# Kernel optimization log

Hardware: AMD Instinct MI355X
Metric: run time of the kernel (lower is better)

## Reference

```python
import jax, jax.numpy as jnp
import numpy as np

NB_HEAD = 16
SIZE_PER_HEAD = 64
D_MODEL = NB_HEAD * SIZE_PER_HEAD  # 1024
B, L = 2, 2048
NEG_BIG = 1e12


def setup_inputs() -> dict:
    key = jax.random.key(0)
    ks = jax.random.split(key, 8)
    return {
        "Q_seq": jax.random.normal(ks[0], (B, L, D_MODEL), dtype=jnp.float32),
        "K_seq": jax.random.normal(ks[1], (B, L, D_MODEL), dtype=jnp.float32),
        "V_seq": jax.random.normal(ks[2], (B, L, D_MODEL), dtype=jnp.float32),
        "q_len": jax.random.randint(ks[3], (B, 1), 1, L, dtype=jnp.int32),
        "v_len": jax.random.randint(ks[4], (B, 1), 1, L, dtype=jnp.int32),
        "WQ": jax.random.normal(ks[5], (D_MODEL, D_MODEL), dtype=jnp.float32) * 0.02,
        "WK": jax.random.normal(ks[6], (D_MODEL, D_MODEL), dtype=jnp.float32) * 0.02,
        "WV": jax.random.normal(ks[7], (D_MODEL, D_MODEL), dtype=jnp.float32) * 0.02,
    }


def _len_mask(lens, length, dtype):
    # Keras code: mask = 1 - cumsum(one_hot(len, L)) -> 1 for pos < len, 0 otherwise
    return (jnp.arange(length)[None, :] < lens).astype(dtype)  # [B, L]


def reference(Q_seq, K_seq, V_seq, q_len, v_len, WQ, WK, WV):
    Bq, Lq, _ = Q_seq.shape
    Lk = K_seq.shape[1]
    # QKV projections, split heads: [B, H, L, D]
    q = (Q_seq @ WQ).reshape(Bq, Lq, NB_HEAD, SIZE_PER_HEAD).transpose(0, 2, 1, 3)
    k = (K_seq @ WK).reshape(Bq, Lk, NB_HEAD, SIZE_PER_HEAD).transpose(0, 2, 1, 3)
    v = (V_seq @ WV).reshape(Bq, Lk, NB_HEAD, SIZE_PER_HEAD).transpose(0, 2, 1, 3)
    # scaled dot-product scores [B, H, Lq, Lk]
    scores = jnp.einsum("bhqd,bhkd->bhqk", q, k) / np.float32(SIZE_PER_HEAD ** 0.5)
    # additive key-length mask (V_len), matching Mask(..., 'add')
    kmask = _len_mask(v_len, Lk, scores.dtype)  # [B, Lk]
    scores = scores - (1.0 - kmask)[:, None, None, :] * np.float32(NEG_BIG)
    A = jax.nn.softmax(scores, axis=-1)
    # attention output, merge heads: [B, Lq, H*D]
    O = jnp.einsum("bhqk,bhkd->bqhd", A, v).reshape(Bq, Lq, D_MODEL)
    # multiplicative query-length mask (Q_len), matching Mask(..., 'mul')
    qmask = _len_mask(q_len, Lq, O.dtype)  # [B, Lq]
    return O * qmask[:, :, None]
```

## Files before the change

kernel.cpp:

```cpp
#include <hip/hip_runtime.h>
#include <cstddef>

#define NB_HEAD 16
#define HEAD_DIM 64
#define D_MODEL 1024
#define BATCH 2
#define SEQ 2048
#define MROWS (BATCH * SEQ)

typedef __bf16 bf16x8 __attribute__((ext_vector_type(8)));
typedef __bf16 bf16x4 __attribute__((ext_vector_type(4)));
typedef float  f32x4  __attribute__((ext_vector_type(4)));

#define XEL ((size_t)MROWS * D_MODEL)
#define WEL ((size_t)D_MODEL * D_MODEL)

static __device__ __forceinline__ size_t xchunk(int row, int k) {
    return ((size_t)(row >> 4) * 32 + (k >> 5)) * 512 + ((k >> 3) & 3) * 128 + (row & 15) * 8 + (k & 7);
}
static __device__ __forceinline__ size_t qkbase(int bh, int row16, int dc) {
    return ((size_t)(bh * 128 + row16) * 2 + dc) * 512;
}
static __device__ __forceinline__ size_t qkelem(int bh, int row, int d) {
    return qkbase(bh, row >> 4, d >> 5) + ((d >> 3) & 3) * 128 + (row & 15) * 8 + (d & 7);
}
static __device__ __forceinline__ size_t vbase(int bh, int d16, int kc) {
    return ((size_t)(bh * 4 + d16) * 64 + kc) * 512;
}
static __device__ __forceinline__ size_t velem(int bh, int d, int key) {
    return vbase(bh, d >> 4, key >> 5) + ((key >> 3) & 3) * 128 + (d & 15) * 8 + (key & 7);
}

static __device__ __forceinline__ void split_bf16(float x, __bf16& h, __bf16& l) {
    h = (__bf16)x;
    l = (__bf16)(x - (float)h);
}

__global__ __launch_bounds__(256) void conv_wt_kernel(
    const float* __restrict__ W0, const float* __restrict__ W1,
    const float* __restrict__ W2,
    __bf16* __restrict__ hi, __bf16* __restrict__ lo)
{
    __shared__ float tile[64][65];
    const int t  = threadIdx.x;
    const int k0 = blockIdx.x * 64;
    const int n0 = blockIdx.y * 64;
    const int z  = blockIdx.z;
    const float* W = (z == 0) ? W0 : ((z == 1) ? W1 : W2);
    __bf16* hz = hi + (size_t)z * WEL;
    __bf16* lz = lo + (size_t)z * WEL;

    #pragma unroll
    for (int p = 0; p < 4; ++p) {
        const int e = (p * 256 + t) * 4;
        const int r = e >> 6, c = e & 63;
        const float4 v = *(const float4*)(W + (size_t)(k0 + r) * D_MODEL + n0 + c);
        tile[r][c] = v.x; tile[r][c + 1] = v.y; tile[r][c + 2] = v.z; tile[r][c + 3] = v.w;
    }
    __syncthreads();
    #pragma unroll
    for (int p = 0; p < 4; ++p) {
        const int e = (p * 256 + t) * 4;
        const int n = e >> 6, kc = e & 63;
        __bf16 h[4], l[4];
        #pragma unroll
        for (int u = 0; u < 4; ++u) split_bf16(tile[kc + u][n], h[u], l[u]);
        const size_t a = xchunk(n0 + n, k0 + kc);
        *(bf16x4*)(hz + a) = (bf16x4){h[0], h[1], h[2], h[3]};
        *(bf16x4*)(lz + a) = (bf16x4){l[0], l[1], l[2], l[3]};
    }
}

__global__ __launch_bounds__(256) void conv_x_kernel(
    const float* __restrict__ X0, const float* __restrict__ X1,
    const float* __restrict__ X2,
    const int* __restrict__ q_len, const int* __restrict__ v_len,
    __bf16* __restrict__ xhi, __bf16* __restrict__ xlo)
{
    const int z = blockIdx.y;
    const size_t e = ((size_t)blockIdx.x * 256 + threadIdx.x) * 8;
    const int l = (int)(e >> 10), k = (int)(e & 1023);
    const int bb = l >> 11, lb = l & (SEQ - 1);
    const int len = (z == 0) ? q_len[bb] : v_len[bb];
    if (lb >= ((len + 127) & ~127)) return;

    const float* X = (z == 0) ? X0 : ((z == 1) ? X1 : X2);
    const float4 v0 = *(const float4*)(X + e);
    const float4 v1 = *(const float4*)(X + e + 4);
    const float xs[8] = {v0.x, v0.y, v0.z, v0.w, v1.x, v1.y, v1.z, v1.w};
    bf16x8 h8, l8;
    #pragma unroll
    for (int u = 0; u < 8; ++u) { __bf16 h_, l_; split_bf16(xs[u], h_, l_); h8[u] = h_; l8[u] = l_; }
    const size_t a = z * XEL + xchunk(l, k);
    *(bf16x8*)(xhi + a) = h8;
    *(bf16x8*)(xlo + a) = l8;
}

__global__ __launch_bounds__(256, 2) void proj_mfma_kernel(
    const __bf16* __restrict__ Xhi, const __bf16* __restrict__ Xlo,
    const __bf16* __restrict__ Wchi, const __bf16* __restrict__ Wclo,
    const int* __restrict__ q_len, const int* __restrict__ v_len,
    __bf16* __restrict__ qch, __bf16* __restrict__ qcl,
    __bf16* __restrict__ kch, __bf16* __restrict__ kcl,
    __bf16* __restrict__ vch, __bf16* __restrict__ vcl)
{
    const int t    = threadIdx.x;
    const int wave = t >> 6, lane = t & 63;
    const int li   = lane & 15, grp = lane >> 4;
    const int wm   = wave >> 1, wn = wave & 1;
    const int m0   = blockIdx.x * 128;
    const int n0   = blockIdx.y * 128;
    const int z    = blockIdx.z;
    const int bb   = m0 >> 11;
    const int l0   = m0 & (SEQ - 1);
    const int need = (z == 0) ? q_len[bb] : v_len[bb];
    if (l0 >= need) return;

    const __bf16* Xh = Xhi + z * XEL;
    const __bf16* Xl = Xlo + z * XEL;
    const __bf16* Wh = Wchi + z * WEL;
    const __bf16* Wl = Wclo + z * WEL;

    const size_t abase = ((size_t)((m0 >> 4) + wm * 4) * 32) * 512 + lane * 8;
    const size_t bbase = ((size_t)((n0 >> 4) + wn * 4) * 32) * 512 + lane * 8;

    f32x4 acc[4][4] = {};
    bf16x8 ah[2][4], al[2][4], bh[2][4], bl[2][4];

    #pragma unroll
    for (int i = 0; i < 4; ++i) {
        ah[0][i] = *(const bf16x8*)(Xh + abase + (size_t)i * 16384);
        al[0][i] = *(const bf16x8*)(Xl + abase + (size_t)i * 16384);
        bh[0][i] = *(const bf16x8*)(Wh + bbase + (size_t)i * 16384);
        bl[0][i] = *(const bf16x8*)(Wl + bbase + (size_t)i * 16384);
    }

    #pragma unroll 2
    for (int kc = 0; kc < 32; ++kc) {
        const int cur = kc & 1, nxt = cur ^ 1;
        if (kc < 31) {
            const size_t ka = abase + (size_t)(kc + 1) * 512;
            const size_t kb = bbase + (size_t)(kc + 1) * 512;
            #pragma unroll
            for (int i = 0; i < 4; ++i) {
                ah[nxt][i] = *(const bf16x8*)(Xh + ka + (size_t)i * 16384);
                al[nxt][i] = *(const bf16x8*)(Xl + ka + (size_t)i * 16384);
                bh[nxt][i] = *(const bf16x8*)(Wh + kb + (size_t)i * 16384);
                bl[nxt][i] = *(const bf16x8*)(Wl + kb + (size_t)i * 16384);
            }
        }
        #pragma unroll
        for (int j = 0; j < 4; ++j) {
            #pragma unroll
            for (int i = 0; i < 4; ++i) {
                acc[i][j] = __builtin_amdgcn_mfma_f32_16x16x32_bf16(ah[cur][i], bh[cur][j], acc[i][j], 0, 0, 0);
                acc[i][j] = __builtin_amdgcn_mfma_f32_16x16x32_bf16(ah[cur][i], bl[cur][j], acc[i][j], 0, 0, 0);
                acc[i][j] = __builtin_amdgcn_mfma_f32_16x16x32_bf16(al[cur][i], bh[cur][j], acc[i][j], 0, 0, 0);
            }
        }
    }

    #pragma unroll
    for (int j = 0; j < 4; ++j) {
        const int cg = n0 + wn * 64 + j * 16 + li;
        const int hd = cg >> 6, d = cg & 63;
        const int bhI = bb * NB_HEAD + hd;
        #pragma unroll
        for (int i = 0; i < 4; ++i) {
            #pragma unroll
            for (int r = 0; r < 4; ++r) {
                const int rg = m0 + wm * 64 + i * 16 + grp * 4 + r;
                const int lg = rg & (SEQ - 1);
                __bf16 h_, l_;
                split_bf16(acc[i][j][r], h_, l_);
                if (z == 0) {
                    const size_t a = qkelem(bhI, lg, d);
                    qch[a] = h_; qcl[a] = l_;
                } else if (z == 1) {
                    const size_t a = qkelem(bhI, lg, d);
                    kch[a] = h_; kcl[a] = l_;
                } else {
                    const size_t a = velem(bhI, d, lg);
                    vch[a] = h_; vcl[a] = l_;
                }
            }
        }
    }
}

__global__ __launch_bounds__(256, 2) void attn_mfma_kernel(
    const __bf16* __restrict__ qch, const __bf16* __restrict__ qcl,
    const __bf16* __restrict__ kch, const __bf16* __restrict__ kcl,
    const __bf16* __restrict__ vch, const __bf16* __restrict__ vcl,
    const int* __restrict__ q_len, const int* __restrict__ v_len,
    float* __restrict__ out)
{
    __shared__ __align__(16) __bf16 Ps[128][72];

    const int t = threadIdx.x;
    const int wq = t >> 6, lane = t & 63;
    const int grp = lane >> 4, li = lane & 15;
    const int hh = blockIdx.x;
    const int q0 = blockIdx.y * 128;
    const int b  = blockIdx.z;
    const int qlen = q_len[b], vlen = v_len[b];
    const int bh = b * NB_HEAD + hh;
    const int qbase = q0 + wq * 32;

    if (qbase >= qlen) {
        const int row = qbase + (lane >> 1), cs = (lane & 1) * 32;
        float* o = out + ((size_t)b * SEQ + row) * D_MODEL + hh * HEAD_DIM + cs;
        const float4 z4 = make_float4(0.f, 0.f, 0.f, 0.f);
        #pragma unroll
        for (int u = 0; u < 8; ++u) *(float4*)(o + u * 4) = z4;
        return;
    }

    bf16x8 qh[2][2], ql[2][2];
    #pragma unroll
    for (int s = 0; s < 2; ++s)
        #pragma unroll
        for (int ks = 0; ks < 2; ++ks) {
            const size_t a = qkbase(bh, (qbase >> 4) + s, ks) + lane * 8;
            qh[s][ks] = *(const bf16x8*)(qch + a);
            ql[s][ks] = *(const bf16x8*)(qcl + a);
        }

    f32x4 O[2][4] = {};
    float m_s[2][4], l_s[2][4];
    #pragma unroll
    for (int s = 0; s < 2; ++s)
        #pragma unroll
        for (int r = 0; r < 4; ++r) { m_s[s][r] = -1e30f; l_s[s][r] = 0.f; }

    const int nkt = (vlen + 63) >> 6;

    for (int tt = 0; tt < nkt; ++tt) {
        const int k0 = tt * 64;

        f32x4 sacc[2][4] = {};
        #pragma unroll
        for (int ks = 0; ks < 2; ++ks) {
            bf16x8 kh_[4], kl_[4];
            #pragma unroll
            for (int j = 0; j < 4; ++j) {
                const size_t a = qkbase(bh, (k0 >> 4) + j, ks) + lane * 8;
                kh_[j] = *(const bf16x8*)(kch + a);
                kl_[j] = *(const bf16x8*)(kcl + a);
            }
            #pragma unroll
            for (int j = 0; j < 4; ++j)
                #pragma unroll
                for (int s = 0; s < 2; ++s) {
                    sacc[s][j] = __builtin_amdgcn_mfma_f32_16x16x32_bf16(qh[s][ks], kh_[j], sacc[s][j], 0, 0, 0);
                    sacc[s][j] = __builtin_amdgcn_mfma_f32_16x16x32_bf16(qh[s][ks], kl_[j], sacc[s][j], 0, 0, 0);
                    sacc[s][j] = __builtin_amdgcn_mfma_f32_16x16x32_bf16(ql[s][ks], kh_[j], sacc[s][j], 0, 0, 0);
                }
        }

        bf16x8 vh_[2][4], vl_[2][4];
        #pragma unroll
        for (int ks = 0; ks < 2; ++ks)
            #pragma unroll
            for (int j = 0; j < 4; ++j) {
                const size_t a = vbase(bh, j, (k0 >> 5) + ks) + lane * 8;
                vh_[ks][j] = *(const bf16x8*)(vch + a);
                vl_[ks][j] = *(const bf16x8*)(vcl + a);
            }

        #pragma unroll
        for (int s = 0; s < 2; ++s) {
            float mx[4] = {-1e30f, -1e30f, -1e30f, -1e30f};
            #pragma unroll
            for (int j = 0; j < 4; ++j) {
                const int key = k0 + j * 16 + li;
                #pragma unroll
                for (int r = 0; r < 4; ++r) {
                    float v = sacc[s][j][r] * 0.125f;
                    if (key >= vlen) v = -1e30f;
                    sacc[s][j][r] = v;
                    mx[r] = fmaxf(mx[r], v);
                }
            }
            #pragma unroll
            for (int r = 0; r < 4; ++r) {
                mx[r] = fmaxf(mx[r], __shfl_xor(mx[r], 1));
                mx[r] = fmaxf(mx[r], __shfl_xor(mx[r], 2));
                mx[r] = fmaxf(mx[r], __shfl_xor(mx[r], 4));
                mx[r] = fmaxf(mx[r], __shfl_xor(mx[r], 8));
            }
            float al[4], sum[4];
            #pragma unroll
            for (int r = 0; r < 4; ++r) {
                const float mn = fmaxf(m_s[s][r], mx[r]);
                al[r] = __expf(m_s[s][r] - mn);
                m_s[s][r] = mn;
                sum[r] = 0.f;
            }
            #pragma unroll
            for (int j = 0; j < 4; ++j)
                #pragma unroll
                for (int r = 0; r < 4; ++r) {
                    const float p = __expf(sacc[s][j][r] - m_s[s][r]);
                    const __bf16 pb = (__bf16)p;
                    sum[r] += (float)pb;
                    Ps[wq * 32 + s * 16 + grp * 4 + r][j * 16 + li] = pb;
                }
            #pragma unroll
            for (int r = 0; r < 4; ++r) {
                sum[r] += __shfl_xor(sum[r], 1);
                sum[r] += __shfl_xor(sum[r], 2);
                sum[r] += __shfl_xor(sum[r], 4);
                sum[r] += __shfl_xor(sum[r], 8);
                l_s[s][r] = l_s[s][r] * al[r] + sum[r];
            }
            #pragma unroll
            for (int j = 0; j < 4; ++j)
                #pragma unroll
                for (int r = 0; r < 4; ++r) O[s][j][r] *= al[r];
        }
        asm volatile("s_waitcnt lgkmcnt(0)" ::: "memory");

        #pragma unroll
        for (int ks = 0; ks < 2; ++ks) {
            bf16x8 pa[2];
            #pragma unroll
            for (int s = 0; s < 2; ++s)
                pa[s] = *(const bf16x8*)&Ps[wq * 32 + s * 16 + li][ks * 32 + grp * 8];
            #pragma unroll
            for (int j = 0; j < 4; ++j)
                #pragma unroll
                for (int s = 0; s < 2; ++s) {
                    O[s][j] = __builtin_amdgcn_mfma_f32_16x16x32_bf16(pa[s], vh_[ks][j], O[s][j], 0, 0, 0);
                    O[s][j] = __builtin_amdgcn_mfma_f32_16x16x32_bf16(pa[s], vl_[ks][j], O[s][j], 0, 0, 0);
                }
        }
    }

    #pragma unroll
    for (int s = 0; s < 2; ++s)
        #pragma unroll
        for (int r = 0; r < 4; ++r) {
            const int q = qbase + s * 16 + grp * 4 + r;
            const float inv = (q < qlen) ? 1.f / l_s[s][r] : 0.f;
            #pragma unroll
            for (int j = 0; j < 4; ++j)
                out[((size_t)b * SEQ + q) * D_MODEL + hh * HEAD_DIM + j * 16 + li] = O[s][j][r] * inv;
        }
}

extern "C" void kernel_launch(void* const* d_in, const int* in_sizes, int n_in,
                              void* d_out, int out_size, void* d_ws, size_t ws_size,
                              hipStream_t stream)
{
    (void)in_sizes; (void)n_in; (void)out_size; (void)ws_size;
    const float* Q_seq = (const float*)d_in[0];
    const float* K_seq = (const float*)d_in[1];
    const float* V_seq = (const float*)d_in[2];
    const int*   q_len = (const int*)d_in[3];
    const int*   v_len = (const int*)d_in[4];
    const float* WQ    = (const float*)d_in[5];
    const float* WK    = (const float*)d_in[6];
    const float* WV    = (const float*)d_in[7];
    float* out = (float*)d_out;

    __bf16* wchi = (__bf16*)d_ws;
    __bf16* wclo = wchi + 3 * WEL;
    __bf16* xhi_ = wclo + 3 * WEL;
    __bf16* xlo_ = xhi_ + 3 * XEL;
    __bf16* qch_ = xlo_ + 3 * XEL;
    __bf16* qcl_ = qch_ + XEL;
    __bf16* kch_ = qcl_ + XEL;
    __bf16* kcl_ = kch_ + XEL;
    __bf16* vch_ = kcl_ + XEL;
    __bf16* vcl_ = vch_ + XEL;

    dim3 blk(256);

    dim3 cg(D_MODEL / 64, D_MODEL / 64, 3);
    conv_wt_kernel<<<cg, blk, 0, stream>>>(WQ, WK, WV, wchi, wclo);

    dim3 xg((unsigned)(XEL / 2048), 3);
    conv_x_kernel<<<xg, blk, 0, stream>>>(Q_seq, K_seq, V_seq, q_len, v_len, xhi_, xlo_);

    dim3 pg(MROWS / 128, D_MODEL / 128, 3);
    proj_mfma_kernel<<<pg, blk, 0, stream>>>(xhi_, xlo_, wchi, wclo, q_len, v_len,
                                             qch_, qcl_, kch_, kcl_, vch_, vcl_);

    dim3 ag(NB_HEAD, SEQ / 128, BATCH);
    attn_mfma_kernel<<<ag, blk, 0, stream>>>(qch_, qcl_, kch_, kcl_, vch_, vcl_,
                                             q_len, v_len, out);
}
```

Measured before the change: 304.5 us.

## Shrink projection M-tile, fold score scale into Q, widen attention key tile

The projection kernel now uses 64-row M tiles with a larger grid and launch bounds that request three blocks per SIMD, which should raise occupancy and parallelism. The 1/sqrt(d) scale moves into the Q projection epilogue, so the attention kernel no longer multiplies every score. The attention kernel processes 128 keys per iteration, skips key masking on full tiles, and loads K/V fragments just in time instead of staging arrays. It also drops the explicit LDS waitcnt, which risks a race on Ps unless the compiler inserts the wait itself.

```diff
diff --git a/kernel.cpp b/kernel.cpp
--- a/kernel.cpp
+++ b/kernel.cpp
@@ -79,7 +79,7 @@
 {
     const int z = blockIdx.y;
     const size_t e = ((size_t)blockIdx.x * 256 + threadIdx.x) * 8;
-    const int l = (int)(e >> 10), k = (int)(e & 1023);
+    const int l = (int)(e >> 10);
     const int bb = l >> 11, lb = l & (SEQ - 1);
     const int len = (z == 0) ? q_len[bb] : v_len[bb];
     if (lb >= ((len + 127) & ~127)) return;
@@ -91,12 +91,12 @@
     bf16x8 h8, l8;
     #pragma unroll
     for (int u = 0; u < 8; ++u) { __bf16 h_, l_; split_bf16(xs[u], h_, l_); h8[u] = h_; l8[u] = l_; }
-    const size_t a = z * XEL + xchunk(l, k);
+    const size_t a = z * XEL + xchunk(l, (int)(e & 1023));
     *(bf16x8*)(xhi + a) = h8;
     *(bf16x8*)(xlo + a) = l8;
 }
 
-__global__ __launch_bounds__(256, 2) void proj_mfma_kernel(
+__global__ __launch_bounds__(256, 3) void proj_mfma_kernel(
     const __bf16* __restrict__ Xhi, const __bf16* __restrict__ Xlo,
     const __bf16* __restrict__ Wchi, const __bf16* __restrict__ Wclo,
     const int* __restrict__ q_len, const int* __restrict__ v_len,
@@ -108,7 +108,7 @@
     const int wave = t >> 6, lane = t & 63;
     const int li   = lane & 15, grp = lane >> 4;
     const int wm   = wave >> 1, wn = wave & 1;
-    const int m0   = blockIdx.x * 128;
+    const int m0   = blockIdx.x * 64;
     const int n0   = blockIdx.y * 128;
     const int z    = blockIdx.z;
     const int bb   = m0 >> 11;
@@ -121,18 +121,21 @@
     const __bf16* Wh = Wchi + z * WEL;
     const __bf16* Wl = Wclo + z * WEL;
 
-    const size_t abase = ((size_t)((m0 >> 4) + wm * 4) * 32) * 512 + lane * 8;
+    const size_t abase = ((size_t)((m0 >> 4) + wm * 2) * 32) * 512 + lane * 8;
     const size_t bbase = ((size_t)((n0 >> 4) + wn * 4) * 32) * 512 + lane * 8;
 
-    f32x4 acc[4][4] = {};
-    bf16x8 ah[2][4], al[2][4], bh[2][4], bl[2][4];
-
-    #pragma unroll
-    for (int i = 0; i < 4; ++i) {
+    f32x4 acc[2][4] = {};
+    bf16x8 ah[2][2], al[2][2], bh[2][4], bl[2][4];
+
+    #pragma unroll
+    for (int i = 0; i < 2; ++i) {
         ah[0][i] = *(const bf16x8*)(Xh + abase + (size_t)i * 16384);
         al[0][i] = *(const bf16x8*)(Xl + abase + (size_t)i * 16384);
-        bh[0][i] = *(const bf16x8*)(Wh + bbase + (size_t)i * 16384);
-        bl[0][i] = *(const bf16x8*)(Wl + bbase + (size_t)i * 16384);
+    }
+    #pragma unroll
+    for (int j = 0; j < 4; ++j) {
+        bh[0][j] = *(const bf16x8*)(Wh + bbase + (size_t)j * 16384);
+        bl[0][j] = *(const bf16x8*)(Wl + bbase + (size_t)j * 16384);
     }
 
     #pragma unroll 2
@@ -142,37 +145,40 @@
             const size_t ka = abase + (size_t)(kc + 1) * 512;
             const size_t kb = bbase + (size_t)(kc + 1) * 512;
             #pragma unroll
-            for (int i = 0; i < 4; ++i) {
+            for (int i = 0; i < 2; ++i) {
                 ah[nxt][i] = *(const bf16x8*)(Xh + ka + (size_t)i * 16384);
                 al[nxt][i] = *(const bf16x8*)(Xl + ka + (size_t)i * 16384);
-                bh[nxt][i] = *(const bf16x8*)(Wh + kb + (size_t)i * 16384);
-                bl[nxt][i] = *(const bf16x8*)(Wl + kb + (size_t)i * 16384);
-            }
-        }
-        #pragma unroll
-        for (int j = 0; j < 4; ++j) {
-            #pragma unroll
-            for (int i = 0; i < 4; ++i) {
+            }
+            #pragma unroll
+            for (int j = 0; j < 4; ++j) {
+                bh[nxt][j] = *(const bf16x8*)(Wh + kb + (size_t)j * 16384);
+                bl[nxt][j] = *(const bf16x8*)(Wl + kb + (size_t)j * 16384);
+            }
+        }
+        #pragma unroll
+        for (int j = 0; j < 4; ++j)
+            #pragma unroll
+            for (int i = 0; i < 2; ++i) {
                 acc[i][j] = __builtin_amdgcn_mfma_f32_16x16x32_bf16(ah[cur][i], bh[cur][j], acc[i][j], 0, 0, 0);
                 acc[i][j] = __builtin_amdgcn_mfma_f32_16x16x32_bf16(ah[cur][i], bl[cur][j], acc[i][j], 0, 0, 0);
                 acc[i][j] = __builtin_amdgcn_mfma_f32_16x16x32_bf16(al[cur][i], bh[cur][j], acc[i][j], 0, 0, 0);
             }
-        }
-    }
-
+    }
+
+    const float oscale = (z == 0) ? 0.125f : 1.0f;
     #pragma unroll
     for (int j = 0; j < 4; ++j) {
         const int cg = n0 + wn * 64 + j * 16 + li;
         const int hd = cg >> 6, d = cg & 63;
         const int bhI = bb * NB_HEAD + hd;
         #pragma unroll
-        for (int i = 0; i < 4; ++i) {
+        for (int i = 0; i < 2; ++i) {
             #pragma unroll
             for (int r = 0; r < 4; ++r) {
-                const int rg = m0 + wm * 64 + i * 16 + grp * 4 + r;
+                const int rg = m0 + wm * 32 + i * 16 + grp * 4 + r;
                 const int lg = rg & (SEQ - 1);
                 __bf16 h_, l_;
-                split_bf16(acc[i][j][r], h_, l_);
+                split_bf16(acc[i][j][r] * oscale, h_, l_);
                 if (z == 0) {
                     const size_t a = qkelem(bhI, lg, d);
                     qch[a] = h_; qcl[a] = l_;
@@ -195,7 +201,7 @@
     const int* __restrict__ q_len, const int* __restrict__ v_len,
     float* __restrict__ out)
 {
-    __shared__ __align__(16) __bf16 Ps[128][72];
+    __shared__ __align__(16) __bf16 Ps[128][132];
 
     const int t = threadIdx.x;
     const int wq = t >> 6, lane = t & 63;
@@ -233,54 +239,49 @@
         #pragma unroll
         for (int r = 0; r < 4; ++r) { m_s[s][r] = -1e30f; l_s[s][r] = 0.f; }
 
-    const int nkt = (vlen + 63) >> 6;
+    const int nkt = (vlen + 127) >> 7;
 
     for (int tt = 0; tt < nkt; ++tt) {
-        const int k0 = tt * 64;
-
-        f32x4 sacc[2][4] = {};
+        const int k0 = tt * 128;
+        const bool full = (k0 + 128 <= vlen);
+
+        f32x4 sacc[2][8] = {};
         #pragma unroll
         for (int ks = 0; ks < 2; ++ks) {
-            bf16x8 kh_[4], kl_[4];
-            #pragma unroll
-            for (int j = 0; j < 4; ++j) {
+            #pragma unroll
+            for (int j = 0; j < 8; ++j) {
                 const size_t a = qkbase(bh, (k0 >> 4) + j, ks) + lane * 8;
-                kh_[j] = *(const bf16x8*)(kch + a);
-                kl_[j] = *(const bf16x8*)(kcl + a);
-            }
-            #pragma unroll
-            for (int j = 0; j < 4; ++j)
+                const bf16x8 kh_ = *(const bf16x8*)(kch + a);
+                const bf16x8 kl_ = *(const bf16x8*)(kcl + a);
                 #pragma unroll
                 for (int s = 0; s < 2; ++s) {
-                    sacc[s][j] = __builtin_amdgcn_mfma_f32_16x16x32_bf16(qh[s][ks], kh_[j], sacc[s][j], 0, 0, 0);
-                    sacc[s][j] = __builtin_amdgcn_mfma_f32_16x16x32_bf16(qh[s][ks], kl_[j], sacc[s][j], 0, 0, 0);
-                    sacc[s][j] = __builtin_amdgcn_mfma_f32_16x16x32_bf16(ql[s][ks], kh_[j], sacc[s][j], 0, 0, 0);
-                }
-        }
-
-        bf16x8 vh_[2][4], vl_[2][4];
-        #pragma unroll
-        for (int ks = 0; ks < 2; ++ks)
-            #pragma unroll
-            for (int j = 0; j < 4; ++j) {
-                const size_t a = vbase(bh, j, (k0 >> 5) + ks) + lane * 8;
-                vh_[ks][j] = *(const bf16x8*)(vch + a);
-                vl_[ks][j] = *(const bf16x8*)(vcl + a);
-            }
+                    sacc[s][j] = __builtin_amdgcn_mfma_f32_16x16x32_bf16(qh[s][ks], kh_, sacc[s][j], 0, 0, 0);
+                    sacc[s][j] = __builtin_amdgcn_mfma_f32_16x16x32_bf16(qh[s][ks], kl_, sacc[s][j], 0, 0, 0);
+                    sacc[s][j] = __builtin_amdgcn_mfma_f32_16x16x32_bf16(ql[s][ks], kh_, sacc[s][j], 0, 0, 0);
+                }
+            }
+        }
 
         #pragma unroll
         for (int s = 0; s < 2; ++s) {
             float mx[4] = {-1e30f, -1e30f, -1e30f, -1e30f};
-            #pragma unroll
-            for (int j = 0; j < 4; ++j) {
-                const int key = k0 + j * 16 + li;
-                #pragma unroll
-                for (int r = 0; r < 4; ++r) {
-                    float v = sacc[s][j][r] * 0.125f;
-                    if (key >= vlen) v = -1e30f;
-                    sacc[s][j][r] = v;
-                    mx[r] = fmaxf(mx[r], v);
-                }
+            if (!full) {
+                #pragma unroll
+                for (int j = 0; j < 8; ++j) {
+                    const int key = k0 + j * 16 + li;
+                    #pragma unroll
+                    for (int r = 0; r < 4; ++r) {
+                        float v = sacc[s][j][r];
+                        if (key >= vlen) v = -1e30f;
+                        sacc[s][j][r] = v;
+                        mx[r] = fmaxf(mx[r], v);
+                    }
+                }
+            } else {
+                #pragma unroll
+                for (int j = 0; j < 8; ++j)
+                    #pragma unroll
+                    for (int r = 0; r < 4; ++r) mx[r] = fmaxf(mx[r], sacc[s][j][r]);
             }
             #pragma unroll
             for (int r = 0; r < 4; ++r) {
@@ -298,7 +299,7 @@
                 sum[r] = 0.f;
             }
             #pragma unroll
-            for (int j = 0; j < 4; ++j)
+            for (int j = 0; j < 8; ++j)
                 #pragma unroll
                 for (int r = 0; r < 4; ++r) {
                     const float p = __expf(sacc[s][j][r] - m_s[s][r]);
@@ -319,21 +320,24 @@
                 #pragma unroll
                 for (int r = 0; r < 4; ++r) O[s][j][r] *= al[r];
         }
-        asm volatile("s_waitcnt lgkmcnt(0)" ::: "memory");
-
-        #pragma unroll
-        for (int ks = 0; ks < 2; ++ks) {
+
+        #pragma unroll
+        for (int ks = 0; ks < 4; ++ks) {
             bf16x8 pa[2];
             #pragma unroll
             for (int s = 0; s < 2; ++s)
                 pa[s] = *(const bf16x8*)&Ps[wq * 32 + s * 16 + li][ks * 32 + grp * 8];
             #pragma unroll
-            for (int j = 0; j < 4; ++j)
+            for (int j = 0; j < 4; ++j) {
+                const size_t a = vbase(bh, j, (k0 >> 5) + ks) + lane * 8;
+                const bf16x8 vh_ = *(const bf16x8*)(vch + a);
+                const bf16x8 vl_ = *(const bf16x8*)(vcl + a);
                 #pragma unroll
                 for (int s = 0; s < 2; ++s) {
-                    O[s][j] = __builtin_amdgcn_mfma_f32_16x16x32_bf16(pa[s], vh_[ks][j], O[s][j], 0, 0, 0);
-                    O[s][j] = __builtin_amdgcn_mfma_f32_16x16x32_bf16(pa[s], vl_[ks][j], O[s][j], 0, 0, 0);
-                }
+                    O[s][j] = __builtin_amdgcn_mfma_f32_16x16x32_bf16(pa[s], vh_, O[s][j], 0, 0, 0);
+                    O[s][j] = __builtin_amdgcn_mfma_f32_16x16x32_bf16(pa[s], vl_, O[s][j], 0, 0, 0);
+                }
+            }
         }
     }
 
@@ -383,7 +387,7 @@
     dim3 xg((unsigned)(XEL / 2048), 3);
     conv_x_kernel<<<xg, blk, 0, stream>>>(Q_seq, K_seq, V_seq, q_len, v_len, xhi_, xlo_);
 
-    dim3 pg(MROWS / 128, D_MODEL / 128, 3);
+    dim3 pg(MROWS / 64, D_MODEL / 128, 3);
     proj_mfma_kernel<<<pg, blk, 0, stream>>>(xhi_, xlo_, wchi, wclo, q_len, v_len,
                                              qch_, qcl_, kch_, kcl_, vch_, vcl_);
 
```

Result: no change. 308.9 us (+1.4%).
